# Kernel optimization log

Hardware: AMD Instinct MI355X
Metric: run time of the kernel (lower is better)

Reference implementation:

```python
import jax, jax.numpy as jnp
import numpy as np

N_NODES = 10000
N_EDGES = 160000
IN_C, HID_C, OUT_C = 256, 512, 256
DROP_P = 0.5


def setup_inputs() -> dict:
    key = jax.random.key(0)
    ks = jax.random.split(key, 6)
    tensor = jax.random.normal(ks[0], (N_NODES, IN_C), dtype=jnp.float32)
    edge_index = jax.random.randint(ks[1], (2, N_EDGES), 0, N_NODES, dtype=jnp.int64)
    # Glorot-ish init for GCNConv linear weights, zero bias (PyG default bias init is zeros)
    W1 = jax.random.normal(ks[2], (IN_C, HID_C), dtype=jnp.float32) * (1.0 / np.sqrt(IN_C))
    b1 = jnp.zeros((HID_C,), dtype=jnp.float32)
    W2 = jax.random.normal(ks[3], (HID_C, OUT_C), dtype=jnp.float32) * (1.0 / np.sqrt(HID_C))
    b2 = jnp.zeros((OUT_C,), dtype=jnp.float32)
    return {"tensor": tensor, "edge_index": edge_index, "W1": W1, "b1": b1, "W2": W2, "b2": b2}


def _gcn_layer(x, W, b, src, dst, n_nodes):
    # x' = D^{-1/2} (A + I) D^{-1/2} X W + b  (PyG GCNConv, add_self_loops=True)
    xw = x @ W                                             # [N, C_out]
    deg = jax.ops.segment_sum(jnp.ones(src.shape[0], xw.dtype), dst,
                              num_segments=n_nodes)        # includes self-loops -> deg >= 1
    dinv = jax.lax.rsqrt(deg)
    norm = dinv[src] * dinv[dst]                           # [E+N]
    msg = xw[src] * norm[:, None]                          # gather + normalize
    out = jax.ops.segment_sum(msg, dst, num_segments=n_nodes)  # scatter-add
    return out + b


def _dropout(x, key, p):
    keep = jax.random.bernoulli(key, 1.0 - p, x.shape)
    return jnp.where(keep, x / (1.0 - p), jnp.zeros((), x.dtype))


def reference(tensor, edge_index, W1, b1, W2, b2):
    n = tensor.shape[0]
    src, dst = edge_index[0], edge_index[1]
    loops = jnp.arange(n, dtype=src.dtype)
    src_f = jnp.concatenate([src, loops])
    dst_f = jnp.concatenate([dst, loops])

    dk1, dk2 = jax.random.split(jax.random.key(42))
    h = _gcn_layer(tensor, W1, b1, src_f, dst_f, n)
    h = jax.nn.relu(h)
    h = _dropout(h, dk1, DROP_P)
    h = _gcn_layer(h, W2, b2, src_f, dst_f, n)
    h = jax.nn.relu(h)
    h = _dropout(h, dk2, DROP_P)
    return h
```

## Files before the change

kernel.cpp:

```cpp
#include <hip/hip_runtime.h>
#include <stdint.h>


#define C_IN 256
#define C_HID 512
#define C_OUT 256

typedef unsigned short ushort_t;
typedef __bf16 bf16x8 __attribute__((ext_vector_type(8)));
typedef float floatx4 __attribute__((ext_vector_type(4)));

typedef __attribute__((address_space(1))) const void g1_void;
typedef __attribute__((address_space(3))) void l3_void;

__device__ __forceinline__ void gll16(const ushort_t* g, ushort_t* l) {
  __builtin_amdgcn_global_load_lds((g1_void*)g, (l3_void*)l, 16, 0, 0);
}

__host__ __device__ __forceinline__ void tf_rounds(unsigned& x0, unsigned& x1,
                                                   unsigned k0, unsigned k1) {
  unsigned k2 = k0 ^ k1 ^ 0x1BD11BDAu;
#define ROT(r) { x0 += x1; x1 = (x1 << r) | (x1 >> (32 - r)); x1 ^= x0; }
  x0 += k0; x1 += k1;
  ROT(13) ROT(15) ROT(26) ROT(6)
  x0 += k1; x1 += k2 + 1u;
  ROT(17) ROT(29) ROT(16) ROT(24)
  x0 += k2; x1 += k0 + 2u;
  ROT(13) ROT(15) ROT(26) ROT(6)
  x0 += k0; x1 += k1 + 3u;
  ROT(17) ROT(29) ROT(16) ROT(24)
  x0 += k1; x1 += k2 + 4u;
  ROT(13) ROT(15) ROT(26) ROT(6)
  x0 += k2; x1 += k0 + 5u;
#undef ROT
}

__device__ __forceinline__ float drop_scale(unsigned j, unsigned k0, unsigned k1) {
  unsigned x0 = 0u, x1 = j;
  tf_rounds(x0, x1, k0, k1);
  unsigned bits = x0 ^ x1;
  float u = __uint_as_float((bits >> 9) | 0x3f800000u) - 1.0f;
  return (u < 0.5f) ? 2.0f : 0.0f;
}

__device__ __forceinline__ ushort_t f2bf(float f) {
  unsigned u = __float_as_uint(f);
  unsigned r = (u + 0x7fffu + ((u >> 16) & 1u)) >> 16;
  return (ushort_t)r;
}
__device__ __forceinline__ float bf2f(ushort_t h) {
  return __uint_as_float(((unsigned)h) << 16);
}

__global__ __launch_bounds__(256) void k_setup(const unsigned* __restrict__ raw,
                                               unsigned* __restrict__ flag,
                                               int* __restrict__ cnt, int N, int NB,
                                               const float* __restrict__ W1,
                                               const float* __restrict__ W2,
                                               ushort_t* __restrict__ h1,
                                               ushort_t* __restrict__ l1,
                                               ushort_t* __restrict__ h2,
                                               ushort_t* __restrict__ l2) {
  int b = blockIdx.x, t = threadIdx.x;
  if (b < NB) {
    int i = b * 256 + t;
    if (i < N) cnt[i] = 0;
    return;
  }
  if (b == NB) {
    __shared__ unsigned sh[256];
    unsigned acc = 0;
    for (int i = 1 + 2 * t; i < 8192; i += 512) acc |= raw[i];
    sh[t] = acc;
    __syncthreads();
    for (int s = 128; s > 0; s >>= 1) {
      if (t < s) sh[t] |= sh[t + s];
      __syncthreads();
    }
    if (t == 0) *flag = (sh[0] == 0u) ? 1u : 0u;
    return;
  }
  int idx = (b - NB - 1) * 256 + t;
  const int S1 = C_IN * C_HID;
  if (idx >= S1 + C_HID * C_OUT) return;
  const float* W; ushort_t *hi, *lo; int K, Nn, li;
  if (idx < S1) { W = W1; hi = h1; lo = l1; K = C_IN; Nn = C_HID; li = idx; }
  else { W = W2; hi = h2; lo = l2; K = C_HID; Nn = C_OUT; li = idx - S1; }
  int k = li / Nn, n = li - k * Nn;
  float v = W[li];
  ushort_t h = f2bf(v);
  hi[(size_t)n * K + k] = h;
  lo[(size_t)n * K + k] = f2bf(v - bf2f(h));
}

__global__ __launch_bounds__(256) void k_hist(const void* __restrict__ raw,
                                              const unsigned* __restrict__ flag,
                                              int* __restrict__ cnt, int E) {
  int e = blockIdx.x * 256 + threadIdx.x;
  if (e >= E) return;
  int d;
  if (*flag) d = (int)((const long long*)raw)[E + e];
  else       d = ((const int*)raw)[E + e];
  atomicAdd(&cnt[d], 1);
}

__global__ __launch_bounds__(1024) void k_scan(const int* __restrict__ cnt,
                                               int* __restrict__ roff,
                                               int* __restrict__ cursor,
                                               float* __restrict__ dinv,
                                               int n, int E) {
  __shared__ int wsum[16];
  __shared__ int sbase;
  int t = threadIdx.x;
  int lane = t & 63, w = t >> 6;
  if (t == 0) sbase = 0;
  __syncthreads();
  for (int c0 = 0; c0 < n; c0 += 1024) {
    int i = c0 + t;
    int v = (i < n) ? cnt[i] : 0;
    int sc = v;
#pragma unroll
    for (int d = 1; d < 64; d <<= 1) {
      int u = __shfl_up(sc, d);
      if (lane >= d) sc += u;
    }
    if (lane == 63) wsum[w] = sc;
    __syncthreads();
    int wpre = 0;
#pragma unroll
    for (int k = 0; k < 16; ++k) wpre += (k < w) ? wsum[k] : 0;
    int base = sbase;
    if (i < n) {
      int excl = base + wpre + sc - v;
      roff[i] = excl;
      cursor[i] = excl;
      dinv[i] = rsqrtf((float)(v + 1));
    }
    __syncthreads();
    if (t == 1023) sbase = base + wpre + sc;
    __syncthreads();
  }
  if (t == 0) roff[n] = E;
}

__global__ __launch_bounds__(256) void k_scatter(const void* __restrict__ raw,
                                                 const unsigned* __restrict__ flag,
                                                 int* __restrict__ cursor,
                                                 int* __restrict__ csr, int E) {
  int e = blockIdx.x * 256 + threadIdx.x;
  if (e >= E) return;
  int s, d;
  if (*flag) {
    s = (int)((const long long*)raw)[e];
    d = (int)((const long long*)raw)[E + e];
  } else {
    s = ((const int*)raw)[e];
    d = ((const int*)raw)[E + e];
  }
  int slot = atomicAdd(&cursor[d], 1);
  csr[slot] = s;
}

template <int EPI, int PRE>
__global__ __launch_bounds__(256) void k_gather4(const int* __restrict__ roff,
                                                 const int* __restrict__ csr,
                                                 const float* __restrict__ dinv,
                                                 const float* __restrict__ x,
                                                 const float* __restrict__ bias,
                                                 void* __restrict__ o1,
                                                 void* __restrict__ o2,
                                                 unsigned dk0, unsigned dk1) {
  int g = threadIdx.x >> 6;
  int tg = threadIdx.x & 63;
  int node = blockIdx.x * 4 + g;
  float dd = dinv[node];
  const float4* xr = (const float4*)x;
  float4 v = xr[(size_t)node * 64 + tg];
  float4 acc;
  if (PRE) acc = v;
  else acc = make_float4(dd * v.x, dd * v.y, dd * v.z, dd * v.w);
  int p = roff[node], end = roff[node + 1];
  int s[8];
  bool have = (p + 8 <= end);
  if (have) {
#pragma unroll
    for (int q = 0; q < 8; ++q) s[q] = csr[p + q];
  }
  while (have) {
    int sn[8];
    bool haven = (p + 16 <= end);
    if (haven) {
#pragma unroll
      for (int q = 0; q < 8; ++q) sn[q] = csr[p + 8 + q];
    }
    float4 r[8];
#pragma unroll
    for (int q = 0; q < 8; ++q) r[q] = xr[(size_t)s[q] * 64 + tg];
    if (PRE) {
#pragma unroll
      for (int q = 0; q < 8; ++q) {
        acc.x += r[q].x; acc.y += r[q].y; acc.z += r[q].z; acc.w += r[q].w;
      }
    } else {
      float w[8];
#pragma unroll
      for (int q = 0; q < 8; ++q) w[q] = dinv[s[q]];
#pragma unroll
      for (int q = 0; q < 8; ++q) {
        acc.x += w[q] * r[q].x; acc.y += w[q] * r[q].y;
        acc.z += w[q] * r[q].z; acc.w += w[q] * r[q].w;
      }
    }
    p += 8;
#pragma unroll
    for (int q = 0; q < 8; ++q) s[q] = sn[q];
    have = haven;
  }
  for (; p + 4 <= end; p += 4) {
    int s0 = csr[p], s1 = csr[p + 1], s2 = csr[p + 2], s3 = csr[p + 3];
    float4 a = xr[(size_t)s0 * 64 + tg];
    float4 b = xr[(size_t)s1 * 64 + tg];
    float4 c = xr[(size_t)s2 * 64 + tg];
    float4 d = xr[(size_t)s3 * 64 + tg];
    if (PRE) {
      acc.x += a.x + b.x + c.x + d.x;
      acc.y += a.y + b.y + c.y + d.y;
      acc.z += a.z + b.z + c.z + d.z;
      acc.w += a.w + b.w + c.w + d.w;
    } else {
      float w0 = dinv[s0], w1 = dinv[s1], w2 = dinv[s2], w3 = dinv[s3];
      acc.x += w0 * a.x + w1 * b.x + w2 * c.x + w3 * d.x;
      acc.y += w0 * a.y + w1 * b.y + w2 * c.y + w3 * d.y;
      acc.z += w0 * a.z + w1 * b.z + w2 * c.z + w3 * d.z;
      acc.w += w0 * a.w + w1 * b.w + w2 * c.w + w3 * d.w;
    }
  }
  for (; p < end; ++p) {
    int s0 = csr[p];
    float4 a = xr[(size_t)s0 * 64 + tg];
    if (PRE) {
      acc.x += a.x; acc.y += a.y; acc.z += a.z; acc.w += a.w;
    } else {
      float w0 = dinv[s0];
      acc.x += w0 * a.x; acc.y += w0 * a.y; acc.z += w0 * a.z; acc.w += w0 * a.w;
    }
  }
  acc.x *= dd; acc.y *= dd; acc.z *= dd; acc.w *= dd;
  if (EPI) {
    float4 bb = ((const float4*)bias)[tg];
    acc.x = fmaxf(acc.x + bb.x, 0.0f);
    acc.y = fmaxf(acc.y + bb.y, 0.0f);
    acc.z = fmaxf(acc.z + bb.z, 0.0f);
    acc.w = fmaxf(acc.w + bb.w, 0.0f);
    unsigned jb = (unsigned)node * 256u + (unsigned)tg * 4u;
    acc.x *= drop_scale(jb + 0u, dk0, dk1);
    acc.y *= drop_scale(jb + 1u, dk0, dk1);
    acc.z *= drop_scale(jb + 2u, dk0, dk1);
    acc.w *= drop_scale(jb + 3u, dk0, dk1);
    ((float4*)o1)[(size_t)node * 64 + tg] = acc;
  } else {
    ushort_t h0 = f2bf(acc.x), h1 = f2bf(acc.y), h2 = f2bf(acc.z), h3 = f2bf(acc.w);
    ushort4 hv = make_ushort4(h0, h1, h2, h3);
    ushort4 lv = make_ushort4(f2bf(acc.x - bf2f(h0)), f2bf(acc.y - bf2f(h1)),
                              f2bf(acc.z - bf2f(h2)), f2bf(acc.w - bf2f(h3)));
    ((ushort4*)o1)[(size_t)node * 64 + tg] = hv;
    ((ushort4*)o2)[(size_t)node * 64 + tg] = lv;
  }
}

__global__ __launch_bounds__(512) void k_gemm12(
    const ushort_t* __restrict__ Ahi, const ushort_t* __restrict__ Alo,
    const ushort_t* __restrict__ B1h, const ushort_t* __restrict__ B1l,
    const ushort_t* __restrict__ B2h, const ushort_t* __restrict__ B2l,
    const float* __restrict__ b1, const float* __restrict__ dinv,
    float* __restrict__ hw2, int M, unsigned dk0, unsigned dk1) {
  __shared__ __attribute__((aligned(16))) ushort_t sA[16384];
  __shared__ __attribute__((aligned(16))) ushort_t sBh[2][4096], sBl[2][4096];
  __shared__ __attribute__((aligned(16))) ushort_t sHh[4096], sHl[4096];
  const int t = threadIdx.x;
  const int lane = t & 63, wave = t >> 6;
  const int wm = wave & 1, wn = wave >> 1;
  const int quad = lane >> 4, l16 = lane & 15;
  const int row0 = blockIdx.x * 32;
  const int skc = (((t & 3) ^ ((t >> 3) & 3)) * 8);
  const int qx8 = (quad ^ ((l16 >> 1) & 3)) * 8;
  const int rs = t >> 2;

  {
    int ch = t & 31;
    int r0a = t >> 5;
#pragma unroll
    for (int seg = 0; seg < 2; ++seg) {
      int row = seg * 16 + r0a;
      int ga = min(row0 + row, M - 1);
      int sc = (ch ^ (row & 7)) * 8;
      gll16(Ahi + (size_t)ga * 256 + sc, &sA[seg * 4096 + t * 8]);
      gll16(Alo + (size_t)ga * 256 + sc, &sA[8192 + seg * 4096 + t * 8]);
    }
  }
#define STG_W1(c, cb, kk8) {                                                  \
    gll16(B1h + ((size_t)(cb) * 128 + rs) * 256 + (kk8) * 32 + skc,           \
          &sBh[c][t * 8]);                                                    \
    gll16(B1l + ((size_t)(cb) * 128 + rs) * 256 + (kk8) * 32 + skc,           \
          &sBl[c][t * 8]); }
#define STG_W2(c, ph, cb, ks2) {                                              \
    gll16(B2h + ((size_t)(ph) * 128 + rs) * 512 + (cb) * 128 + (ks2) * 32 + skc, \
          &sBh[c][t * 8]);                                                    \
    gll16(B2l + ((size_t)(ph) * 128 + rs) * 512 + (cb) * 128 + (ks2) * 32 + skc, \
          &sBl[c][t * 8]); }

  STG_W1(0, 0, 0)
  asm volatile("s_waitcnt vmcnt(0)\n\ts_barrier" ::: "memory");

  floatx4 acc2[4] = {};
  int c = 0;
  const int rA = wm * 16 + l16;
  for (int cb = 0; cb < 4; ++cb) {
    floatx4 acc1[2] = {};
    for (int kk8 = 0; kk8 < 8; ++kk8) {
      if (kk8 < 7) { STG_W1(c ^ 1, cb, kk8 + 1) }
      else { STG_W2(c ^ 1, 0, cb, 0) }
      asm volatile("s_waitcnt vmcnt(2)\n\ts_barrier" ::: "memory");
      const int offA = rA * 256 + (((kk8 * 4 + quad) ^ (rA & 7)) * 8);
      bf16x8 ah = *(const bf16x8*)&sA[offA];
      bf16x8 al = *(const bf16x8*)&sA[8192 + offA];
#pragma unroll
      for (int j = 0; j < 2; ++j) {
        const int offB = (wn * 32 + j * 16 + l16) * 32 + qx8;
        bf16x8 bh = *(const bf16x8*)&sBh[c][offB];
        bf16x8 bl = *(const bf16x8*)&sBl[c][offB];
        acc1[j] = __builtin_amdgcn_mfma_f32_16x16x32_bf16(ah, bh, acc1[j], 0, 0, 0);
        acc1[j] = __builtin_amdgcn_mfma_f32_16x16x32_bf16(ah, bl, acc1[j], 0, 0, 0);
        acc1[j] = __builtin_amdgcn_mfma_f32_16x16x32_bf16(al, bh, acc1[j], 0, 0, 0);
      }
      asm volatile("s_barrier" ::: "memory");
      c ^= 1;
    }
#pragma unroll
    for (int j = 0; j < 2; ++j) {
      int kc = wn * 32 + j * 16 + l16;
      int gc = cb * 128 + kc;
      float bb = b1[gc];
#pragma unroll
      for (int reg = 0; reg < 4; ++reg) {
        int row = wm * 16 + quad * 4 + reg;
        float v = acc1[j][reg] + bb;
        v = fmaxf(v, 0.0f);
        v *= drop_scale((unsigned)(row0 + row) * 512u + (unsigned)gc, dk0, dk1);
        ushort_t h = f2bf(v);
        int idx = row * 128 + (((kc >> 3) ^ (row & 7)) * 8) + (kc & 7);
        sHh[idx] = h;
        sHl[idx] = f2bf(v - bf2f(h));
      }
    }
    asm volatile("s_waitcnt lgkmcnt(0)\n\ts_barrier" ::: "memory");
#pragma unroll
    for (int s2 = 0; s2 < 8; ++s2) {
      const int ph = s2 >> 2, ks2 = s2 & 3;
      if (s2 < 7) { STG_W2(c ^ 1, (s2 + 1) >> 2, cb, (s2 + 1) & 3) }
      else if (cb < 3) { STG_W1(c ^ 1, cb + 1, 0) }
      if (s2 < 7 || cb < 3) {
        asm volatile("s_waitcnt vmcnt(2)\n\ts_barrier" ::: "memory");
      } else {
        asm volatile("s_waitcnt vmcnt(0)\n\ts_barrier" ::: "memory");
      }
      const int offA = rA * 128 + (((ks2 * 4 + quad) ^ (rA & 7)) * 8);
      bf16x8 ah = *(const bf16x8*)&sHh[offA];
      bf16x8 al = *(const bf16x8*)&sHl[offA];
#pragma unroll
      for (int j = 0; j < 2; ++j) {
        const int offB = (wn * 32 + j * 16 + l16) * 32 + qx8;
        bf16x8 bh = *(const bf16x8*)&sBh[c][offB];
        bf16x8 bl = *(const bf16x8*)&sBl[c][offB];
        acc2[ph * 2 + j] = __builtin_amdgcn_mfma_f32_16x16x32_bf16(ah, bh, acc2[ph * 2 + j], 0, 0, 0);
        acc2[ph * 2 + j] = __builtin_amdgcn_mfma_f32_16x16x32_bf16(ah, bl, acc2[ph * 2 + j], 0, 0, 0);
        acc2[ph * 2 + j] = __builtin_amdgcn_mfma_f32_16x16x32_bf16(al, bh, acc2[ph * 2 + j], 0, 0, 0);
      }
      asm volatile("s_barrier" ::: "memory");
      c ^= 1;
    }
  }
#undef STG_W1
#undef STG_W2
#pragma unroll
  for (int ph = 0; ph < 2; ++ph) {
#pragma unroll
    for (int j = 0; j < 2; ++j) {
      int gc = ph * 128 + wn * 32 + j * 16 + l16;
#pragma unroll
      for (int reg = 0; reg < 4; ++reg) {
        int gr = row0 + wm * 16 + quad * 4 + reg;
        if (gr < M) hw2[(size_t)gr * 256 + gc] = acc2[ph * 2 + j][reg] * dinv[gr];
      }
    }
  }
}

extern "C" void kernel_launch(void* const* d_in, const int* in_sizes, int n_in,
                              void* d_out, int out_size, void* d_ws, size_t ws_size,
                              hipStream_t stream) {
  const float* x  = (const float*)d_in[0];
  const void*  ei = d_in[1];
  const float* W1 = (const float*)d_in[2];
  const float* b1 = (const float*)d_in[3];
  const float* W2 = (const float*)d_in[4];
  const float* b2 = (const float*)d_in[5];
  float* out = (float*)d_out;

  const int N = in_sizes[0] / C_IN;
  const int E = in_sizes[1] / 2;
  const int NB = (N + 255) / 256;

  unsigned a0 = 0u, a1 = 0u, b0 = 0u, b1k = 1u;
  tf_rounds(a0, a1, 0u, 42u);
  tf_rounds(b0, b1k, 0u, 42u);

  uintptr_t base = (uintptr_t)d_ws;
  unsigned*  flag   = (unsigned*)base;
  int*       cnt    = (int*)(base + 16 * 1024);
  int*       roff   = (int*)(base + 64 * 1024);
  int*       cursor = (int*)(base + 128 * 1024);
  float*     dinv   = (float*)(base + 192 * 1024);
  int*       csr    = (int*)(base + 2u * 1024 * 1024);
  ushort_t*  Ahi    = (ushort_t*)(base + 4u  * 1024 * 1024);
  ushort_t*  Alo    = (ushort_t*)(base + 10u * 1024 * 1024);
  float*     hw2    = (float*)(base + 38u * 1024 * 1024);
  ushort_t*  W1thi  = (ushort_t*)(base + 49u * 1024 * 1024);
  ushort_t*  W1tlo  = (ushort_t*)(base + 49u * 1024 * 1024 + 512 * 1024);
  ushort_t*  W2thi  = (ushort_t*)(base + 50u * 1024 * 1024);
  ushort_t*  W2tlo  = (ushort_t*)(base + 50u * 1024 * 1024 + 512 * 1024);

  dim3 b256(256);
  const int WCB = (C_IN * C_HID + C_HID * C_OUT + 255) / 256;

  k_setup<<<dim3(NB + 1 + WCB), b256, 0, stream>>>((const unsigned*)ei, flag, cnt,
                                                   N, NB, W1, W2,
                                                   W1thi, W1tlo, W2thi, W2tlo);
  k_hist<<<dim3((E + 255) / 256), b256, 0, stream>>>(ei, flag, cnt, E);
  k_scan<<<dim3(1), dim3(1024), 0, stream>>>(cnt, roff, cursor, dinv, N, E);
  k_scatter<<<dim3((E + 255) / 256), b256, 0, stream>>>(ei, flag, cursor, csr, E);
  k_gather4<0, 0><<<dim3(N / 4), b256, 0, stream>>>(roff, csr, dinv, x, nullptr,
                                                    Ahi, Alo, 0u, 0u);
  k_gemm12<<<dim3((N + 31) / 32), dim3(512), 0, stream>>>(
      Ahi, Alo, W1thi, W1tlo, W2thi, W2tlo, b1, dinv, hw2, N, a0, a1);
  k_gather4<1, 1><<<dim3(N / 4), b256, 0, stream>>>(roff, csr, dinv, hw2, b2,
                                                    out, nullptr, b0, b1k);
}
```

Baseline: 201.0 us.

## Restructure fused GEMM to 4 waves with register-resident A and wider K stages

The fused two-layer GEMM kernel drops from 512 to 256 threads per block, with each wave now computing 64 output columns instead of 32. The A-operand (hi/lo bf16 of the aggregated input) is loaded straight into registers instead of staged through LDS, and the bias is prefetched. Weight tiles are staged 64 K-elements at a time, halving the number of barrier-separated steps. This cuts LDS traffic and synchronisation per MFMA in exchange for much higher register pressure. That pressure could limit occupancy despite the launch bound of two blocks.

```diff
diff --git a/kernel.cpp b/kernel.cpp
--- a/kernel.cpp
+++ b/kernel.cpp
@@ -268,84 +268,96 @@
   }
 }
 
-__global__ __launch_bounds__(512) void k_gemm12(
+__global__ __launch_bounds__(256, 2) void k_gemm12(
     const ushort_t* __restrict__ Ahi, const ushort_t* __restrict__ Alo,
     const ushort_t* __restrict__ B1h, const ushort_t* __restrict__ B1l,
     const ushort_t* __restrict__ B2h, const ushort_t* __restrict__ B2l,
     const float* __restrict__ b1, const float* __restrict__ dinv,
     float* __restrict__ hw2, int M, unsigned dk0, unsigned dk1) {
-  __shared__ __attribute__((aligned(16))) ushort_t sA[16384];
-  __shared__ __attribute__((aligned(16))) ushort_t sBh[2][4096], sBl[2][4096];
+  __shared__ __attribute__((aligned(16))) ushort_t sBh[2][8192], sBl[2][8192];
   __shared__ __attribute__((aligned(16))) ushort_t sHh[4096], sHl[4096];
   const int t = threadIdx.x;
   const int lane = t & 63, wave = t >> 6;
   const int wm = wave & 1, wn = wave >> 1;
   const int quad = lane >> 4, l16 = lane & 15;
   const int row0 = blockIdx.x * 32;
-  const int skc = (((t & 3) ^ ((t >> 3) & 3)) * 8);
-  const int qx8 = (quad ^ ((l16 >> 1) & 3)) * 8;
-  const int rs = t >> 2;
-
+  const int rA = wm * 16 + l16;
+
+  bf16x8 Ah[8], Al[8];
   {
-    int ch = t & 31;
-    int r0a = t >> 5;
-#pragma unroll
-    for (int seg = 0; seg < 2; ++seg) {
-      int row = seg * 16 + r0a;
-      int ga = min(row0 + row, M - 1);
-      int sc = (ch ^ (row & 7)) * 8;
-      gll16(Ahi + (size_t)ga * 256 + sc, &sA[seg * 4096 + t * 8]);
-      gll16(Alo + (size_t)ga * 256 + sc, &sA[8192 + seg * 4096 + t * 8]);
-    }
-  }
-#define STG_W1(c, cb, kk8) {                                                  \
-    gll16(B1h + ((size_t)(cb) * 128 + rs) * 256 + (kk8) * 32 + skc,           \
-          &sBh[c][t * 8]);                                                    \
-    gll16(B1l + ((size_t)(cb) * 128 + rs) * 256 + (kk8) * 32 + skc,           \
-          &sBl[c][t * 8]); }
-#define STG_W2(c, ph, cb, ks2) {                                              \
-    gll16(B2h + ((size_t)(ph) * 128 + rs) * 512 + (cb) * 128 + (ks2) * 32 + skc, \
-          &sBh[c][t * 8]);                                                    \
-    gll16(B2l + ((size_t)(ph) * 128 + rs) * 512 + (cb) * 128 + (ks2) * 32 + skc, \
-          &sBl[c][t * 8]); }
-
-  STG_W1(0, 0, 0)
+    const int ga = min(row0 + rA, M - 1);
+    const ushort_t* pa = Ahi + (size_t)ga * 256 + quad * 8;
+    const ushort_t* pl = Alo + (size_t)ga * 256 + quad * 8;
+#pragma unroll
+    for (int k8 = 0; k8 < 8; ++k8) {
+      Ah[k8] = *(const bf16x8*)(pa + k8 * 32);
+      Al[k8] = *(const bf16x8*)(pl + k8 * 32);
+    }
+  }
+  float bpre[4][4];
+#pragma unroll
+  for (int cb = 0; cb < 4; ++cb)
+#pragma unroll
+    for (int j = 0; j < 4; ++j)
+      bpre[cb][j] = b1[cb * 128 + wn * 64 + j * 16 + l16];
+#pragma unroll
+  for (int k8 = 0; k8 < 8; ++k8)
+    asm volatile("" :: "v"(Ah[k8]), "v"(Al[k8]));
+#pragma unroll
+  for (int cb = 0; cb < 4; ++cb)
+    asm volatile("" :: "v"(bpre[cb][0]), "v"(bpre[cb][1]),
+                       "v"(bpre[cb][2]), "v"(bpre[cb][3]));
+
+#define STG(bh_, bl_, Kd_, colb_, kb_, c_) {                                   \
+    _Pragma("unroll")                                                          \
+    for (int i_ = 0; i_ < 4; ++i_) {                                           \
+      int slab_ = wave * 4 + i_;                                               \
+      int row_ = slab_ * 8 + (lane >> 3);                                      \
+      int kch_ = (((lane & 7) ^ (row_ & 7)) * 8);                              \
+      gll16(bh_ + (size_t)(colb_ + row_) * Kd_ + (kb_) + kch_,                 \
+            &sBh[c_][slab_ * 512]);                                            \
+      gll16(bl_ + (size_t)(colb_ + row_) * Kd_ + (kb_) + kch_,                 \
+            &sBl[c_][slab_ * 512]);                                            \
+    } }
+
+  STG(B1h, B1l, 256, 0, 0, 0)
   asm volatile("s_waitcnt vmcnt(0)\n\ts_barrier" ::: "memory");
 
-  floatx4 acc2[4] = {};
+  floatx4 acc2[2][4] = {};
   int c = 0;
-  const int rA = wm * 16 + l16;
   for (int cb = 0; cb < 4; ++cb) {
-    floatx4 acc1[2] = {};
-    for (int kk8 = 0; kk8 < 8; ++kk8) {
-      if (kk8 < 7) { STG_W1(c ^ 1, cb, kk8 + 1) }
-      else { STG_W2(c ^ 1, 0, cb, 0) }
-      asm volatile("s_waitcnt vmcnt(2)\n\ts_barrier" ::: "memory");
-      const int offA = rA * 256 + (((kk8 * 4 + quad) ^ (rA & 7)) * 8);
-      bf16x8 ah = *(const bf16x8*)&sA[offA];
-      bf16x8 al = *(const bf16x8*)&sA[8192 + offA];
-#pragma unroll
-      for (int j = 0; j < 2; ++j) {
-        const int offB = (wn * 32 + j * 16 + l16) * 32 + qx8;
-        bf16x8 bh = *(const bf16x8*)&sBh[c][offB];
-        bf16x8 bl = *(const bf16x8*)&sBl[c][offB];
-        acc1[j] = __builtin_amdgcn_mfma_f32_16x16x32_bf16(ah, bh, acc1[j], 0, 0, 0);
-        acc1[j] = __builtin_amdgcn_mfma_f32_16x16x32_bf16(ah, bl, acc1[j], 0, 0, 0);
-        acc1[j] = __builtin_amdgcn_mfma_f32_16x16x32_bf16(al, bh, acc1[j], 0, 0, 0);
+    floatx4 acc1[4] = {};
+#pragma unroll
+    for (int k2 = 0; k2 < 4; ++k2) {
+      if (k2 < 3) { STG(B1h, B1l, 256, cb * 128, (k2 + 1) * 64, c ^ 1) }
+      else        { STG(B2h, B2l, 512, 0, cb * 128, c ^ 1) }
+      asm volatile("s_waitcnt vmcnt(8)\n\ts_barrier" ::: "memory");
+#pragma unroll
+      for (int kk = 0; kk < 2; ++kk) {
+        bf16x8 ah = Ah[k2 * 2 + kk], al = Al[k2 * 2 + kk];
+#pragma unroll
+        for (int j = 0; j < 4; ++j) {
+          int rb = wn * 64 + j * 16 + l16;
+          int ob = rb * 64 + (((kk * 4 + quad) ^ (rb & 7)) * 8);
+          bf16x8 bh = *(const bf16x8*)&sBh[c][ob];
+          bf16x8 bl = *(const bf16x8*)&sBl[c][ob];
+          acc1[j] = __builtin_amdgcn_mfma_f32_16x16x32_bf16(ah, bh, acc1[j], 0, 0, 0);
+          acc1[j] = __builtin_amdgcn_mfma_f32_16x16x32_bf16(ah, bl, acc1[j], 0, 0, 0);
+          acc1[j] = __builtin_amdgcn_mfma_f32_16x16x32_bf16(al, bh, acc1[j], 0, 0, 0);
+        }
       }
       asm volatile("s_barrier" ::: "memory");
       c ^= 1;
     }
 #pragma unroll
-    for (int j = 0; j < 2; ++j) {
-      int kc = wn * 32 + j * 16 + l16;
+    for (int j = 0; j < 4; ++j) {
+      int kc = wn * 64 + j * 16 + l16;
       int gc = cb * 128 + kc;
-      float bb = b1[gc];
+      float bb = bpre[cb][j];
 #pragma unroll
       for (int reg = 0; reg < 4; ++reg) {
         int row = wm * 16 + quad * 4 + reg;
-        float v = acc1[j][reg] + bb;
-        v = fmaxf(v, 0.0f);
+        float v = fmaxf(acc1[j][reg] + bb, 0.0f);
         v *= drop_scale((unsigned)(row0 + row) * 512u + (unsigned)gc, dk0, dk1);
         ushort_t h = f2bf(v);
         int idx = row * 128 + (((kc >> 3) ^ (row & 7)) * 8) + (kc & 7);
@@ -354,43 +366,55 @@
       }
     }
     asm volatile("s_waitcnt lgkmcnt(0)\n\ts_barrier" ::: "memory");
-#pragma unroll
-    for (int s2 = 0; s2 < 8; ++s2) {
-      const int ph = s2 >> 2, ks2 = s2 & 3;
-      if (s2 < 7) { STG_W2(c ^ 1, (s2 + 1) >> 2, cb, (s2 + 1) & 3) }
-      else if (cb < 3) { STG_W1(c ^ 1, cb + 1, 0) }
-      if (s2 < 7 || cb < 3) {
-        asm volatile("s_waitcnt vmcnt(2)\n\ts_barrier" ::: "memory");
+    bf16x8 hh[4], hl[4];
+#pragma unroll
+    for (int kc2 = 0; kc2 < 4; ++kc2) {
+      int oh = rA * 128 + (((kc2 * 4 + quad) ^ (rA & 7)) * 8);
+      hh[kc2] = *(const bf16x8*)&sHh[oh];
+      hl[kc2] = *(const bf16x8*)&sHl[oh];
+    }
+#pragma unroll
+    for (int s2 = 0; s2 < 4; ++s2) {
+      const int ph = s2 >> 1, kk2 = s2 & 1;
+      bool staged = true;
+      if (s2 < 3) {
+        const int sn = s2 + 1;
+        STG(B2h, B2l, 512, (sn >> 1) * 128, cb * 128 + (sn & 1) * 64, c ^ 1)
+      } else if (cb < 3) {
+        STG(B1h, B1l, 256, (cb + 1) * 128, 0, c ^ 1)
       } else {
-        asm volatile("s_waitcnt vmcnt(0)\n\ts_barrier" ::: "memory");
-      }
-      const int offA = rA * 128 + (((ks2 * 4 + quad) ^ (rA & 7)) * 8);
-      bf16x8 ah = *(const bf16x8*)&sHh[offA];
-      bf16x8 al = *(const bf16x8*)&sHl[offA];
-#pragma unroll
-      for (int j = 0; j < 2; ++j) {
-        const int offB = (wn * 32 + j * 16 + l16) * 32 + qx8;
-        bf16x8 bh = *(const bf16x8*)&sBh[c][offB];
-        bf16x8 bl = *(const bf16x8*)&sBl[c][offB];
-        acc2[ph * 2 + j] = __builtin_amdgcn_mfma_f32_16x16x32_bf16(ah, bh, acc2[ph * 2 + j], 0, 0, 0);
-        acc2[ph * 2 + j] = __builtin_amdgcn_mfma_f32_16x16x32_bf16(ah, bl, acc2[ph * 2 + j], 0, 0, 0);
-        acc2[ph * 2 + j] = __builtin_amdgcn_mfma_f32_16x16x32_bf16(al, bh, acc2[ph * 2 + j], 0, 0, 0);
+        staged = false;
+      }
+      if (staged) asm volatile("s_waitcnt vmcnt(8)\n\ts_barrier" ::: "memory");
+      else        asm volatile("s_waitcnt vmcnt(0)\n\ts_barrier" ::: "memory");
+#pragma unroll
+      for (int kk = 0; kk < 2; ++kk) {
+        bf16x8 ah = hh[kk2 * 2 + kk], al = hl[kk2 * 2 + kk];
+#pragma unroll
+        for (int j = 0; j < 4; ++j) {
+          int rb = wn * 64 + j * 16 + l16;
+          int ob = rb * 64 + (((kk * 4 + quad) ^ (rb & 7)) * 8);
+          bf16x8 bh = *(const bf16x8*)&sBh[c][ob];
+          bf16x8 bl = *(const bf16x8*)&sBl[c][ob];
+          acc2[ph][j] = __builtin_amdgcn_mfma_f32_16x16x32_bf16(ah, bh, acc2[ph][j], 0, 0, 0);
+          acc2[ph][j] = __builtin_amdgcn_mfma_f32_16x16x32_bf16(ah, bl, acc2[ph][j], 0, 0, 0);
+          acc2[ph][j] = __builtin_amdgcn_mfma_f32_16x16x32_bf16(al, bh, acc2[ph][j], 0, 0, 0);
+        }
       }
       asm volatile("s_barrier" ::: "memory");
       c ^= 1;
     }
   }
-#undef STG_W1
-#undef STG_W2
+#undef STG
 #pragma unroll
   for (int ph = 0; ph < 2; ++ph) {
 #pragma unroll
-    for (int j = 0; j < 2; ++j) {
-      int gc = ph * 128 + wn * 32 + j * 16 + l16;
+    for (int j = 0; j < 4; ++j) {
+      int gc = ph * 128 + wn * 64 + j * 16 + l16;
 #pragma unroll
       for (int reg = 0; reg < 4; ++reg) {
         int gr = row0 + wm * 16 + quad * 4 + reg;
-        if (gr < M) hw2[(size_t)gr * 256 + gc] = acc2[ph * 2 + j][reg] * dinv[gr];
+        if (gr < M) hw2[(size_t)gr * 256 + gc] = acc2[ph][j][reg] * dinv[gr];
       }
     }
   }
@@ -441,7 +465,7 @@
   k_scatter<<<dim3((E + 255) / 256), b256, 0, stream>>>(ei, flag, cursor, csr, E);
   k_gather4<0, 0><<<dim3(N / 4), b256, 0, stream>>>(roff, csr, dinv, x, nullptr,
                                                     Ahi, Alo, 0u, 0u);
-  k_gemm12<<<dim3((N + 31) / 32), dim3(512), 0, stream>>>(
+  k_gemm12<<<dim3((N + 31) / 32), b256, 0, stream>>>(
       Ahi, Alo, W1thi, W1tlo, W2thi, W2tlo, b1, dinv, hw2, N, a0, a1);
   k_gather4<1, 1><<<dim3(N / 4), b256, 0, stream>>>(roff, csr, dinv, hw2, b2,
                                                     out, nullptr, b0, b1k);
```

Result: slower. 205.7 us (+2.3%).
